# Kernel optimization log

Measured on AMD Instinct MI355X. Metric: run time of the kernel, lower is better.

Reference implementation:

```python
import jax, jax.numpy as jnp
import numpy as np

B, T, C = 4, 2048, 2048
H = 16
D = C // H  # 128


def setup_inputs() -> dict:
    key = jax.random.key(0)
    k1, k2, k3, k4 = jax.random.split(key, 4)
    x = jax.random.normal(k1, (B, T, C), dtype=jnp.float32)
    rope_freqs = jax.random.uniform(k2, (D // 2,), dtype=jnp.float32)
    # torch Linear weights: (out_features, in_features)
    W_attn = jax.random.normal(k3, (3 * C, C), dtype=jnp.float32) * (1.0 / np.sqrt(C))
    W_proj = jax.random.normal(k4, (C, C), dtype=jnp.float32) * (1.0 / np.sqrt(C))
    return {"x": x, "rope_freqs": rope_freqs, "W_attn": W_attn, "W_proj": W_proj}


def _apply_rope(q, k, rope_freqs):
    # q, k: (B, H, T, D); rope_freqs: (D//2,)
    S = q.shape[2]
    positions = jnp.arange(S, dtype=q.dtype)[:, None]            # (S, 1)
    theta = positions * rope_freqs[None, :]                       # (S, D//2)
    sin_t = jnp.sin(theta)[None, None]                            # (1,1,S,D//2)
    cos_t = jnp.cos(theta)[None, None]
    q1, q2 = q[..., 0::2], q[..., 1::2]
    k1, k2 = k[..., 0::2], k[..., 1::2]
    q_out = jnp.concatenate([q1 * cos_t - q2 * sin_t, q1 * sin_t + q2 * cos_t], axis=-1)
    k_out = jnp.concatenate([k1 * cos_t - k2 * sin_t, k1 * sin_t + k2 * cos_t], axis=-1)
    return q_out, k_out


def reference(x, rope_freqs, W_attn, W_proj):
    b, t, c = x.shape
    qkv = jnp.einsum('btc,fc->btf', x, W_attn)                    # (B,T,3C)
    q, k, v = jnp.split(qkv, 3, axis=-1)
    q = q.reshape(b, t, H, D).transpose(0, 2, 1, 3)               # (B,H,T,D)
    k = k.reshape(b, t, H, D).transpose(0, 2, 1, 3)
    v = v.reshape(b, t, H, D).transpose(0, 2, 1, 3)
    q, k = _apply_rope(q, k, rope_freqs)
    scale = 1.0 / jnp.sqrt(jnp.asarray(D, dtype=x.dtype))
    scores = jnp.einsum('bhqd,bhkd->bhqk', q, k) * scale          # (B,H,T,T)
    causal = jnp.tril(jnp.ones((t, t), dtype=bool))
    scores = jnp.where(causal[None, None], scores, jnp.asarray(-jnp.inf, dtype=scores.dtype))
    probs = jax.nn.softmax(scores, axis=-1)
    y = jnp.einsum('bhqk,bhkd->bhqd', probs, v)                   # (B,H,T,D)
    y = y.transpose(0, 2, 1, 3).reshape(b, t, c)
    return jnp.einsum('btc,fc->btf', y, W_proj)
```

## Files before the change

### kernel.cpp

```cpp
#include <hip/hip_runtime.h>
#include <cstdint>
#include <cstddef>


typedef unsigned short u16;
typedef u16    u16x8 __attribute__((ext_vector_type(8)));
typedef __bf16 bf16x8 __attribute__((ext_vector_type(8)));
typedef float  f32x4 __attribute__((ext_vector_type(4)));

#define MFMA16(a, b, c) __builtin_amdgcn_mfma_f32_16x16x32_bf16( \
    __builtin_bit_cast(bf16x8, (a)), __builtin_bit_cast(bf16x8, (b)), (c), 0, 0, 0)

static __device__ __forceinline__ u16 f2b(float f) {
  unsigned u = __builtin_bit_cast(unsigned, f);
  unsigned r = (u + 0x7FFFu + ((u >> 16) & 1u)) >> 16;
  return (u16)r;
}

static __device__ __forceinline__ void gld_lds16(const void* g, void* l) {
  __builtin_amdgcn_global_load_lds(
      (__attribute__((address_space(1))) unsigned int*)(void*)(g),
      (__attribute__((address_space(3))) unsigned int*)(l),
      16, 0, 0);
}

#define BARRIER() asm volatile("s_barrier" ::: "memory")
#define LGKM0()   do { asm volatile("s_waitcnt lgkmcnt(0)" ::: "memory"); \
                       __builtin_amdgcn_sched_barrier(0); } while (0)
#define WAIT_VM(n) asm volatile("s_waitcnt vmcnt(" #n ")" ::: "memory")

__global__ __launch_bounds__(256) void cvt_bf16(const float4* __restrict__ src,
                                                u16x8* __restrict__ dst, int n8) {
  int i = blockIdx.x * 256 + threadIdx.x;
  if (i >= n8) return;
  float4 a = src[i * 2], b = src[i * 2 + 1];
  u16x8 o;
  o[0] = f2b(a.x); o[1] = f2b(a.y); o[2] = f2b(a.z); o[3] = f2b(a.w);
  o[4] = f2b(b.x); o[5] = f2b(b.y); o[6] = f2b(b.z); o[7] = f2b(b.w);
  dst[i] = o;
}

static __device__ __forceinline__ void rdA(u16x8 (&af)[4][2], const u16* p,
                                           int cx0, int cx1) {
#pragma unroll
  for (int i = 0; i < 4; ++i) {
    af[i][0] = *(const u16x8*)(p + i * 1024 + cx0);
    af[i][1] = *(const u16x8*)(p + i * 1024 + cx1);
  }
}

static __device__ __forceinline__ void rdB(u16x8 (&bf)[2][2], const u16* p,
                                           int cx0, int cx1) {
#pragma unroll
  for (int j = 0; j < 2; ++j) {
    bf[j][0] = *(const u16x8*)(p + j * 1024 + cx0);
    bf[j][1] = *(const u16x8*)(p + j * 1024 + cx1);
  }
}

static __device__ __forceinline__ void mm16(f32x4 (&acc)[8][4], int ib, int jb,
                                            const u16x8 (&af)[4][2],
                                            const u16x8 (&bf)[2][2]) {
#pragma unroll
  for (int i = 0; i < 4; ++i)
#pragma unroll
    for (int j = 0; j < 2; ++j) {
      acc[ib + i][jb + j] = MFMA16(af[i][0], bf[j][0], acc[ib + i][jb + j]);
      acc[ib + i][jb + j] = MFMA16(af[i][1], bf[j][1], acc[ib + i][jb + j]);
    }
}

static __device__ __forceinline__ void gemm256_main(
    const u16* __restrict__ A, const u16* __restrict__ Bw, int K,
    int m0, int n0, u16* sm, f32x4 (&acc)[8][4]) {
  const int tid = threadIdx.x;
  const int lane = tid & 63, wv = tid >> 6;
  const int quad = lane >> 4, col = lane & 15;
  const int wm = wv >> 2, wn = wv & 3;

  u16* LA0 = sm;
  u16* LB0 = sm + 16384;
  u16* LA1 = sm + 32768;
  u16* LB1 = sm + 49152;

#pragma unroll
  for (int i = 0; i < 8; ++i)
#pragma unroll
    for (int j = 0; j < 4; ++j) acc[i][j] = (f32x4){0.f, 0.f, 0.f, 0.f};

  const int r8 = lane >> 3, ch = lane & 7;
  const int sc8 = (ch ^ r8) << 3;
  const u16 *aS[4], *bS[4];
  int dof[4];
#pragma unroll
  for (int u = 0; u < 4; ++u) {
    int row = u * 64 + wv * 8 + r8;
    aS[u] = A + (size_t)(m0 + row) * K + sc8;
    bS[u] = Bw + (size_t)(n0 + row) * K + sc8;
    dof[u] = (u * 64 + wv * 8) * 64;
  }

  const int cx0 = ((quad) ^ (col & 7)) << 3;
  const int cx1 = ((4 | quad) ^ (col & 7)) << 3;
  const int offA = (wm * 128 + col) * 64;
  const int offB = (wn * 64 + col) * 64;

  gld_lds16(bS[0], LB0 + dof[0]); gld_lds16(bS[1], LB0 + dof[1]);
  gld_lds16(bS[2], LB0 + dof[2]); gld_lds16(bS[3], LB0 + dof[3]);
  gld_lds16(aS[0], LA0 + dof[0]); gld_lds16(aS[2], LA0 + dof[2]);
  gld_lds16(aS[1], LA0 + dof[1]); gld_lds16(aS[3], LA0 + dof[3]);
  WAIT_VM(2);
  BARRIER();

  u16x8 af[4][2], bfL[2][2], bfH[2][2];
  const int nIt = K >> 7;
#pragma unroll 1
  for (int it = 0; it < nIt; ++it) {
    const size_t ko = (size_t)it * 128 + 64;
    const size_t kn = (size_t)it * 128 + 128;
    const bool hn = (it + 1 < nIt);

    rdA(af, LA0 + offA, cx0, cx1);
    rdB(bfL, LB0 + offB, cx0, cx1);
    gld_lds16(bS[0] + ko, LB1 + dof[0]); gld_lds16(bS[1] + ko, LB1 + dof[1]);
    BARRIER(); LGKM0();
    __builtin_amdgcn_s_setprio(1); mm16(acc, 0, 0, af, bfL);
    __builtin_amdgcn_s_setprio(0);
    BARRIER();
    rdB(bfH, LB0 + offB + 2048, cx0, cx1);
    gld_lds16(bS[2] + ko, LB1 + dof[2]); gld_lds16(bS[3] + ko, LB1 + dof[3]);
    WAIT_VM(4);
    BARRIER(); LGKM0();
    __builtin_amdgcn_s_setprio(1); mm16(acc, 0, 2, af, bfH);
    __builtin_amdgcn_s_setprio(0);
    BARRIER();
    rdA(af, LA0 + offA + 4096, cx0, cx1);
    gld_lds16(aS[0] + ko, LA1 + dof[0]); gld_lds16(aS[2] + ko, LA1 + dof[2]);
    BARRIER(); LGKM0();
    __builtin_amdgcn_s_setprio(1); mm16(acc, 4, 0, af, bfL);
    __builtin_amdgcn_s_setprio(0);
    BARRIER();
    gld_lds16(aS[1] + ko, LA1 + dof[1]); gld_lds16(aS[3] + ko, LA1 + dof[3]);
    WAIT_VM(2);
    BARRIER(); __builtin_amdgcn_sched_barrier(0);
    __builtin_amdgcn_s_setprio(1); mm16(acc, 4, 2, af, bfH);
    __builtin_amdgcn_s_setprio(0);
    BARRIER();
    rdA(af, LA1 + offA, cx0, cx1);
    rdB(bfL, LB1 + offB, cx0, cx1);
    if (hn) { gld_lds16(bS[0] + kn, LB0 + dof[0]); gld_lds16(bS[1] + kn, LB0 + dof[1]); }
    BARRIER(); LGKM0();
    __builtin_amdgcn_s_setprio(1); mm16(acc, 0, 0, af, bfL);
    __builtin_amdgcn_s_setprio(0);
    BARRIER();
    rdB(bfH, LB1 + offB + 2048, cx0, cx1);
    if (hn) {
      gld_lds16(bS[2] + kn, LB0 + dof[2]); gld_lds16(bS[3] + kn, LB0 + dof[3]);
      WAIT_VM(4);
    } else {
      WAIT_VM(0);
    }
    BARRIER(); LGKM0();
    __builtin_amdgcn_s_setprio(1); mm16(acc, 0, 2, af, bfH);
    __builtin_amdgcn_s_setprio(0);
    BARRIER();
    rdA(af, LA1 + offA + 4096, cx0, cx1);
    if (hn) { gld_lds16(aS[0] + kn, LA0 + dof[0]); gld_lds16(aS[2] + kn, LA0 + dof[2]); }
    BARRIER(); LGKM0();
    __builtin_amdgcn_s_setprio(1); mm16(acc, 4, 0, af, bfL);
    __builtin_amdgcn_s_setprio(0);
    BARRIER();
    if (hn) { gld_lds16(aS[1] + kn, LA0 + dof[1]); gld_lds16(aS[3] + kn, LA0 + dof[3]); }
    WAIT_VM(2);
    BARRIER(); __builtin_amdgcn_sched_barrier(0);
    __builtin_amdgcn_s_setprio(1); mm16(acc, 4, 2, af, bfH);
    __builtin_amdgcn_s_setprio(0);
    BARRIER();
  }
}

__global__ __launch_bounds__(512, 2) void gemm_qkv(
    const u16* __restrict__ A, const u16* __restrict__ Bw,
    const float* __restrict__ freqs, int K,
    u16* __restrict__ Qp, u16* __restrict__ Kp, u16* __restrict__ Vp) {
  extern __shared__ u16 sm[];
  const int bid = blockIdx.x;
  const int x = bid & 7, o = bid >> 3;
  const int rnd = o >> 5, w = o & 31;
  const int m0 = (x * 4 + (w & 3)) * 256;
  const int n0 = (rnd * 8 + (w >> 2)) * 256;

  f32x4 acc[8][4];
  gemm256_main(A, Bw, K, m0, n0, sm, acc);

  const int tid = threadIdx.x;
  const int lane = tid & 63, wv = tid >> 6;
  const int quad = lane >> 4, col = lane & 15;
  const int wm = wv >> 2, wn = wv & 3;

  const int which = n0 >> 11;
  const int h0 = (n0 & 2047) >> 7;
  const int b = m0 >> 11, t0 = m0 & 2047;
  const int hl = wn >> 1;

  __syncthreads();

  if (which == 2) {
#pragma unroll
    for (int j = 0; j < 4; ++j) {
      int d = (wn & 1) * 64 + j * 16 + col;
      int key = (d >> 1) & 7;
#pragma unroll
      for (int i = 0; i < 8; ++i)
#pragma unroll
        for (int r = 0; r < 4; ++r) {
          int tgl = wm * 128 + i * 16 + quad * 4 + r;
          int reg = hl * 4 + (tgl >> 6);
          int tc = tgl & 63;
          sm[reg * 8192 + d * 64 + (((tc >> 3) ^ key) << 3) + (tc & 7)] =
              f2b(acc[i][j][r]);
        }
    }
    __syncthreads();
#pragma unroll
    for (int s = 0; s < 16; ++s) {
      int cch = tid + (s << 9);
      int reg = cch >> 10, ci = cch & 1023;
      int d = ci >> 3, cc = ci & 7;
      u16x8 v = *(const u16x8*)(sm + reg * 8192 + d * 64 +
                                (((cc ^ ((d >> 1) & 7))) << 3));
      int hh = reg >> 2, ktg = reg & 3;
      int kt = (t0 >> 6) + ktg;
      size_t off = (((size_t)((b * 16 + h0 + hh) * 32 + kt)) << 13) +
                   (size_t)d * 64 + (cc << 3);
      *(u16x8*)(Vp + off) = v;
    }
  } else {
    u16* dst = (which == 0) ? Qp : Kp;
    const bool evenlane = (col & 1) == 0;
    const int rlo = evenlane ? 0 : 2;
#pragma unroll
    for (int j = 0; j < 4; ++j) {
      int dd = (wn & 1) * 64 + j * 16 + col;
      int jj = dd >> 1;
      float fr = freqs[jj];
#pragma unroll
      for (int i = 0; i < 8; ++i) {
        float oth[4];
#pragma unroll
        for (int r = 0; r < 4; ++r) oth[r] = __shfl_xor(acc[i][j][r], 1);
#pragma unroll
        for (int rr = 0; rr < 2; ++rr) {
          int r = rlo + rr;
          float q1 = evenlane ? acc[i][j][r] : oth[r];
          float q2 = evenlane ? oth[r] : acc[i][j][r];
          int tgl = wm * 128 + i * 16 + quad * 4 + r;
          int t = t0 + tgl;
          float theta = (float)t * fr;
          float rev = theta * 0.15915494309189535f;
          rev -= floorf(rev);
          float sn = __builtin_amdgcn_sinf(rev);
          float cs = __builtin_amdgcn_cosf(rev);
          unsigned pk = (unsigned)f2b(q1 * cs - q2 * sn) |
                        ((unsigned)f2b(q1 * sn + q2 * cs) << 16);
          int row = hl * 256 + tgl;
          int sc = (jj >> 2) ^ (row & 15);
          *(unsigned*)(sm + row * 128 + (sc << 3) + 2 * (jj & 3)) = pk;
        }
      }
    }
    __syncthreads();
#pragma unroll
    for (int s = 0; s < 16; ++s) {
      int cch = tid + (s << 9);
      int row = cch >> 4, cc = cch & 15;
      u16x8 v = *(const u16x8*)(sm + row * 128 + ((cc ^ (row & 15)) << 3));
      int hh = row >> 8, tl = row & 255;
      size_t off = ((size_t)((b * 16 + h0 + hh) * 2048 + t0 + tl)) * 128 +
                   (cc << 3);
      *(u16x8*)(dst + off) = v;
    }
  }
}

__global__ __launch_bounds__(512, 2) void gemm_proj(
    const u16* __restrict__ A, const u16* __restrict__ Bw,
    int N, int K, float* __restrict__ out) {
  extern __shared__ u16 sm[];
  const int bid = blockIdx.x;
  const int x = bid & 7, w = bid >> 3;
  const int m0 = (x * 4 + (w & 3)) * 256;
  const int n0 = (w >> 2) * 256;

  f32x4 acc[8][4];
  gemm256_main(A, Bw, K, m0, n0, sm, acc);

  const int tid = threadIdx.x;
  const int lane = tid & 63, wv = tid >> 6;
  const int quad = lane >> 4, col = lane & 15;
  const int wm = wv >> 2, wn = wv & 3;

#pragma unroll
  for (int i = 0; i < 8; ++i) {
    int mg = m0 + wm * 128 + i * 16 + quad * 4;
#pragma unroll
    for (int j = 0; j < 4; ++j) {
      int ng = n0 + wn * 64 + j * 16 + col;
#pragma unroll
      for (int r = 0; r < 4; ++r) out[(size_t)(mg + r) * N + ng] = acc[i][j][r];
    }
  }
}

__global__ __launch_bounds__(512, 4) void fattn(
    const u16* __restrict__ Qb, const u16* __restrict__ Kb, const u16* __restrict__ Vt,
    u16* __restrict__ Yb) {
  extern __shared__ u16 smem[];
  u16* lP = smem + 32768 + (threadIdx.x >> 6) * 1024;

  const int tid = threadIdx.x;
  const int lane = tid & 63, wv = tid >> 6;
  const int quad = lane >> 4, col = lane & 15;
  const int bh = blockIdx.x;
  const int p = blockIdx.y;
  const int b = bh >> 4, h = bh & 15;
  const size_t base = (size_t)bh << 18;
  const float kcomb = 0.08838834764831845f * 1.4426950408889634f;

#pragma unroll 1
  for (int phase = 0; phase < 2; ++phase) {
    const int tq = phase ? (15 - p) : p;
    const int qr0 = tq * 128 + wv * 16;
    const int dkt = qr0 >> 6;

    u16x8 qf[4];
#pragma unroll
    for (int t = 0; t < 4; ++t)
      qf[t] = *(const u16x8*)(Qb + base + (size_t)(qr0 + col) * 128 + t * 32 + quad * 8);

    f32x4 mrow = (f32x4){-1e30f, -1e30f, -1e30f, -1e30f};
    f32x4 lrow = (f32x4){0.f, 0.f, 0.f, 0.f};
    f32x4 o[8];
#pragma unroll
    for (int dt = 0; dt < 8; ++dt) o[dt] = (f32x4){0.f, 0.f, 0.f, 0.f};

    const int nkt = 2 * tq + 2;

#define FA_STAGE(KT, BI)                                                        \
    do {                                                                        \
      if (wv < 4) {                                                             \
        u16* lkd = smem + (BI) * 8192;                                          \
        _Pragma("unroll")                                                       \
        for (int u = 0; u < 4; ++u) {                                           \
          int row = wv * 16 + u * 4 + (lane >> 4);                              \
          int sc = (lane & 15) ^ (row & 15);                                    \
          gld_lds16(Kb + base + (size_t)((KT) * 64 + row) * 128 + (sc << 3),    \
                    lkd + (size_t)(wv * 16 + u * 4) * 128);                     \
        }                                                                       \
      } else {                                                                  \
        int vw = wv - 4;                                                        \
        u16* lvd = smem + 16384 + (BI) * 8192;                                  \
        const u16* vbase = Vt + ((size_t)(bh * 32 + (KT)) << 13);               \
        _Pragma("unroll")                                                       \
        for (int u = 0; u < 4; ++u) {                                           \
          int row = vw * 32 + u * 8 + (lane >> 3);                              \
          int sc = (lane & 7) ^ (row & 7);                                      \
          gld_lds16(vbase + (size_t)row * 64 + (sc << 3),                       \
                    lvd + (size_t)(vw * 32 + u * 8) * 64);                      \
        }                                                                       \
      }                                                                         \
    } while (0)

    FA_STAGE(0, 0);
    WAIT_VM(0);
    BARRIER();

#pragma unroll 1
    for (int kt = 0; kt < nkt; ++kt) {
      const int cur = kt & 1;
      if (kt + 1 < nkt) {
        FA_STAGE(kt + 1, cur ^ 1);
        WAIT_VM(4);
      } else {
        WAIT_VM(0);
      }
      BARRIER();

      if (kt <= dkt) {
        const u16* lK = smem + cur * 8192;
        const u16* lVt = smem + 16384 + cur * 8192;
        f32x4 sv[4];
#pragma unroll
        for (int nt = 0; nt < 4; ++nt) {
          f32x4 s = (f32x4){0.f, 0.f, 0.f, 0.f};
#pragma unroll
          for (int t = 0; t < 4; ++t) {
            int krow = nt * 16 + col;
            u16x8 kf = *(const u16x8*)&lK[krow * 128 + ((((t << 2) | quad) ^ (krow & 15)) << 3)];
            s = MFMA16(qf[t], kf, s);
          }
          sv[nt] = s;
        }
#pragma unroll
        for (int nt = 0; nt < 4; ++nt)
#pragma unroll
          for (int r = 0; r < 4; ++r) sv[nt][r] *= kcomb;
        if (kt == dkt) {
#pragma unroll
          for (int nt = 0; nt < 4; ++nt) {
            int cg = kt * 64 + nt * 16 + col;
#pragma unroll
            for (int r = 0; r < 4; ++r)
              if (cg > qr0 + quad * 4 + r) sv[nt][r] = -1e30f;
          }
        }
        f32x4 mx = sv[0];
#pragma unroll
        for (int nt = 1; nt < 4; ++nt)
#pragma unroll
          for (int r = 0; r < 4; ++r) mx[r] = fmaxf(mx[r], sv[nt][r]);
#pragma unroll
        for (int off = 1; off < 16; off <<= 1)
#pragma unroll
          for (int r = 0; r < 4; ++r) mx[r] = fmaxf(mx[r], __shfl_xor(mx[r], off));
        f32x4 alpha;
#pragma unroll
        for (int r = 0; r < 4; ++r) {
          float mn = fmaxf(mrow[r], mx[r]);
          alpha[r] = exp2f(mrow[r] - mn);
          mrow[r] = mn;
        }
        f32x4 ps = (f32x4){0.f, 0.f, 0.f, 0.f};
#pragma unroll
        for (int nt = 0; nt < 4; ++nt)
#pragma unroll
          for (int r = 0; r < 4; ++r) {
            float pe = exp2f(sv[nt][r] - mrow[r]);
            ps[r] += pe;
            int row = quad * 4 + r;
            int chn = ((nt << 1) | (col >> 3)) ^ (row & 7);
            lP[row * 64 + (chn << 3) + (col & 7)] = f2b(pe);
          }
#pragma unroll
        for (int off = 1; off < 16; off <<= 1)
#pragma unroll
          for (int r = 0; r < 4; ++r) ps[r] += __shfl_xor(ps[r], off);
#pragma unroll
        for (int r = 0; r < 4; ++r) lrow[r] = lrow[r] * alpha[r] + ps[r];
#pragma unroll
        for (int dt = 0; dt < 8; ++dt)
#pragma unroll
          for (int r = 0; r < 4; ++r) o[dt][r] *= alpha[r];
#pragma unroll
        for (int t = 0; t < 2; ++t) {
          u16x8 pf = *(const u16x8*)&lP[col * 64 + ((((t << 2) | quad) ^ (col & 7)) << 3)];
#pragma unroll
          for (int dt = 0; dt < 8; ++dt) {
            int drow = dt * 16 + col;
            u16x8 vf = *(const u16x8*)&lVt[drow * 64 + ((((t << 2) | quad) ^ (drow & 7)) << 3)];
            o[dt] = MFMA16(pf, vf, o[dt]);
          }
        }
      }
      BARRIER();
    }

    f32x4 inv;
#pragma unroll
    for (int r = 0; r < 4; ++r) inv[r] = 1.0f / lrow[r];
#pragma unroll
    for (int dt = 0; dt < 8; ++dt)
#pragma unroll
      for (int r = 0; r < 4; ++r) {
        float y = o[dt][r] * inv[r];
        int q = qr0 + quad * 4 + r;
        Yb[((size_t)(b * 2048 + q)) * 2048 + h * 128 + dt * 16 + col] = f2b(y);
      }
  }
#undef FA_STAGE
}

extern "C" void kernel_launch(void* const* d_in, const int* in_sizes, int n_in,
                              void* d_out, int out_size, void* d_ws, size_t ws_size,
                              hipStream_t stream) {
  (void)in_sizes; (void)n_in; (void)out_size; (void)ws_size;
  const float* x     = (const float*)d_in[0];
  const float* freqs = (const float*)d_in[1];
  const float* Wattn = (const float*)d_in[2];
  const float* Wproj = (const float*)d_in[3];
  float* out = (float*)d_out;
  char* ws = (char*)d_ws;

  u16* Wq_b = (u16*)(ws + 0);
  u16* Wp_b = (u16*)(ws + 25165824);
  u16* x_b  = (u16*)(ws + 33554432);
  u16* Qb   = (u16*)(ws + 67108864);
  u16* Kb   = (u16*)(ws + 100663296);
  u16* Vt   = (u16*)(ws + 134217728);
  u16* Yb   = (u16*)(ws + 167772160);

  static bool attr_done = false;
  if (!attr_done) {
    (void)hipFuncSetAttribute((const void*)gemm_qkv,
                              hipFuncAttributeMaxDynamicSharedMemorySize, 131072);
    (void)hipFuncSetAttribute((const void*)gemm_proj,
                              hipFuncAttributeMaxDynamicSharedMemorySize, 131072);
    (void)hipFuncSetAttribute((const void*)fattn,
                              hipFuncAttributeMaxDynamicSharedMemorySize, 81920);
    attr_done = true;
  }

  cvt_bf16<<<6144, 256, 0, stream>>>((const float4*)Wattn, (u16x8*)Wq_b, 12582912 / 8);
  cvt_bf16<<<2048, 256, 0, stream>>>((const float4*)Wproj, (u16x8*)Wp_b, 4194304 / 8);
  cvt_bf16<<<8192, 256, 0, stream>>>((const float4*)x, (u16x8*)x_b, 16777216 / 8);

  gemm_qkv<<<dim3(768), 512, 131072, stream>>>(x_b, Wq_b, freqs, 2048, Qb, Kb, Vt);
  fattn<<<dim3(64, 8), 512, 81920, stream>>>(Qb, Kb, Vt, Yb);
  gemm_proj<<<dim3(256), 512, 131072, stream>>>(Yb, Wp_b, 2048, 2048, out);
}
```

Before: 606.5 us.

## Pack V epilogue stores, precompute fattn load offsets, simplify proj grid mapping

The V-transpose epilogue in the QKV GEMM now packs pairs of bf16 values into 32-bit LDS stores, and a barrier before that epilogue is removed. The flash-attention K/V staging macro now uses per-thread source and LDS offsets computed once, which removes address arithmetic and branching from the inner loop. The projection GEMM switches from a swizzled 1D block mapping to a plain 2D grid. Dropping the barrier risks an LDS race if the GEMM main loop does not end with a sync, and the new grid mapping may change L2 reuse.

```diff
diff --git a/kernel.cpp b/kernel.cpp
--- a/kernel.cpp
+++ b/kernel.cpp
@@ -203,7 +203,6 @@
   const int b = m0 >> 11, t0 = m0 & 2047;
   const int hl = wn >> 1;
 
-  __syncthreads();
 
   if (which == 2) {
 #pragma unroll
@@ -211,15 +210,16 @@
       int d = (wn & 1) * 64 + j * 16 + col;
       int key = (d >> 1) & 7;
 #pragma unroll
-      for (int i = 0; i < 8; ++i)
-#pragma unroll
-        for (int r = 0; r < 4; ++r) {
-          int tgl = wm * 128 + i * 16 + quad * 4 + r;
-          int reg = hl * 4 + (tgl >> 6);
-          int tc = tgl & 63;
-          sm[reg * 8192 + d * 64 + (((tc >> 3) ^ key) << 3) + (tc & 7)] =
-              f2b(acc[i][j][r]);
-        }
+      for (int i = 0; i < 8; ++i) {
+        int tbase = wm * 128 + i * 16 + quad * 4;
+        int reg = hl * 4 + (tbase >> 6);
+        int tc0 = tbase & 63;
+        u16* d0 = sm + reg * 8192 + d * 64 + ((((tc0 >> 3) ^ key)) << 3) + (tc0 & 7);
+        *(unsigned*)d0 = (unsigned)f2b(acc[i][j][0]) |
+                         ((unsigned)f2b(acc[i][j][1]) << 16);
+        *(unsigned*)(d0 + 2) = (unsigned)f2b(acc[i][j][2]) |
+                               ((unsigned)f2b(acc[i][j][3]) << 16);
+      }
     }
     __syncthreads();
 #pragma unroll
@@ -287,10 +287,7 @@
     const u16* __restrict__ A, const u16* __restrict__ Bw,
     int N, int K, float* __restrict__ out) {
   extern __shared__ u16 sm[];
-  const int bid = blockIdx.x;
-  const int x = bid & 7, w = bid >> 3;
-  const int m0 = (x * 4 + (w & 3)) * 256;
-  const int n0 = (w >> 2) * 256;
+  const int m0 = blockIdx.y * 256, n0 = blockIdx.x * 256;
 
   f32x4 acc[8][4];
   gemm256_main(A, Bw, K, m0, n0, sm, acc);
@@ -327,6 +324,40 @@
   const size_t base = (size_t)bh << 18;
   const float kcomb = 0.08838834764831845f * 1.4426950408889634f;
 
+  const u16* srcBase;
+  u16* ldsBase;
+  int so[4], lo[4];
+  if (wv < 4) {
+    srcBase = Kb + base;
+    ldsBase = smem;
+#pragma unroll
+    for (int u = 0; u < 4; ++u) {
+      int row = wv * 16 + u * 4 + (lane >> 4);
+      int sc = (lane & 15) ^ (row & 15);
+      so[u] = row * 128 + (sc << 3);
+      lo[u] = (wv * 16 + u * 4) * 128;
+    }
+  } else {
+    int vw = wv - 4;
+    srcBase = Vt + base;
+    ldsBase = smem + 16384;
+#pragma unroll
+    for (int u = 0; u < 4; ++u) {
+      int row = vw * 32 + u * 8 + (lane >> 3);
+      int sc = (lane & 7) ^ (row & 7);
+      so[u] = row * 64 + (sc << 3);
+      lo[u] = (vw * 32 + u * 8) * 64;
+    }
+  }
+
+#define FA_STAGE(KT, BI)                                                        \
+    do {                                                                        \
+      const u16* s_ = srcBase + (size_t)(KT) * 8192;                            \
+      u16* d_ = ldsBase + (BI) * 8192;                                          \
+      gld_lds16(s_ + so[0], d_ + lo[0]); gld_lds16(s_ + so[1], d_ + lo[1]);     \
+      gld_lds16(s_ + so[2], d_ + lo[2]); gld_lds16(s_ + so[3], d_ + lo[3]);     \
+    } while (0)
+
 #pragma unroll 1
   for (int phase = 0; phase < 2; ++phase) {
     const int tq = phase ? (15 - p) : p;
@@ -345,31 +376,6 @@
     for (int dt = 0; dt < 8; ++dt) o[dt] = (f32x4){0.f, 0.f, 0.f, 0.f};
 
     const int nkt = 2 * tq + 2;
-
-#define FA_STAGE(KT, BI)                                                        \
-    do {                                                                        \
-      if (wv < 4) {                                                             \
-        u16* lkd = smem + (BI) * 8192;                                          \
-        _Pragma("unroll")                                                       \
-        for (int u = 0; u < 4; ++u) {                                           \
-          int row = wv * 16 + u * 4 + (lane >> 4);                              \
-          int sc = (lane & 15) ^ (row & 15);                                    \
-          gld_lds16(Kb + base + (size_t)((KT) * 64 + row) * 128 + (sc << 3),    \
-                    lkd + (size_t)(wv * 16 + u * 4) * 128);                     \
-        }                                                                       \
-      } else {                                                                  \
-        int vw = wv - 4;                                                        \
-        u16* lvd = smem + 16384 + (BI) * 8192;                                  \
-        const u16* vbase = Vt + ((size_t)(bh * 32 + (KT)) << 13);               \
-        _Pragma("unroll")                                                       \
-        for (int u = 0; u < 4; ++u) {                                           \
-          int row = vw * 32 + u * 8 + (lane >> 3);                              \
-          int sc = (lane & 7) ^ (row & 7);                                      \
-          gld_lds16(vbase + (size_t)row * 64 + (sc << 3),                       \
-                    lvd + (size_t)(vw * 32 + u * 8) * 64);                      \
-        }                                                                       \
-      }                                                                         \
-    } while (0)
 
     FA_STAGE(0, 0);
     WAIT_VM(0);
@@ -516,5 +522,5 @@
 
   gemm_qkv<<<dim3(768), 512, 131072, stream>>>(x_b, Wq_b, freqs, 2048, Qb, Kb, Vt);
   fattn<<<dim3(64, 8), 512, 81920, stream>>>(Qb, Kb, Vt, Yb);
-  gemm_proj<<<dim3(256), 512, 131072, stream>>>(Yb, Wp_b, 2048, 2048, out);
-}
+  gemm_proj<<<dim3(8, 32), 512, 131072, stream>>>(Yb, Wp_b, 2048, 2048, out);
+}
```

Result: faster. 585.8 us (-3.4%).
